# Kernel optimization log

Hardware: AMD Instinct MI355X
Metric: run time of the kernel (lower is better)

Reference implementation:

```python
import jax, jax.numpy as jnp
import numpy as np

N, E, D, H, C = 40000, 640000, 128, 4, 32  # nodes, edges, in_hid, heads, out_channels/head
NUM_NODE_TYPE, NUM_EDGE_TYPE = 8, 8
NEG_SLOPE = 0.2
EDGE_TYPE_SELF = 0


def setup_inputs() -> dict:
    key = jax.random.key(0)
    ks = jax.random.split(key, 12)
    x = jax.random.normal(ks[0], (N, D), dtype=jnp.float32)
    # build edges with no self-loops (the module filters src==dst before adding self-loops)
    src = jax.random.randint(ks[1], (E,), 0, N, dtype=jnp.int32)
    off = jax.random.randint(ks[2], (E,), 1, N, dtype=jnp.int32)
    dst = (src + off) % N
    edge_index = jnp.stack([src, dst])  # [2, E]
    node_type = jax.random.randint(ks[3], (N,), 0, NUM_NODE_TYPE, dtype=jnp.int32)
    edge_type = jax.random.randint(ks[4], (E,), 0, NUM_EDGE_TYPE, dtype=jnp.int32)
    g = 0.05
    Wq = jax.random.normal(ks[5], (H * C, D), dtype=jnp.float32) * g
    Wk = jax.random.normal(ks[6], (H * C, D), dtype=jnp.float32) * g
    Wv = jax.random.normal(ks[7], (H * C, D), dtype=jnp.float32) * g
    att_i = jax.random.normal(ks[8], (1, H, C), dtype=jnp.float32) * g
    att_j = jax.random.normal(ks[9], (1, H, C), dtype=jnp.float32) * g
    bias = jnp.zeros((H * C,), dtype=jnp.float32)
    node_emb_table = jax.random.normal(ks[10], (NUM_NODE_TYPE, D), dtype=jnp.float32) * g
    edge_emb_table = jax.random.normal(ks[11], (NUM_EDGE_TYPE, D), dtype=jnp.float32) * g
    return {"x": x, "edge_index": edge_index, "node_type": node_type,
            "edge_type": edge_type, "Wq": Wq, "Wk": Wk, "Wv": Wv,
            "att_i": att_i, "att_j": att_j, "bias": bias,
            "node_emb_table": node_emb_table, "edge_emb_table": edge_emb_table}


def reference(x, edge_index, node_type, edge_type, Wq, Wk, Wv,
              att_i, att_j, bias, node_emb_table, edge_emb_table):
    n = x.shape[0]
    # node-type embedding add
    x = x + node_emb_table[node_type]                       # [N, D]
    xq = x @ Wq.T                                           # [N, H*C]
    # add self-loops (input edges contain no src==dst by construction)
    self_idx = jnp.arange(n, dtype=edge_index.dtype)
    src = jnp.concatenate([edge_index[0], self_idx])        # [E+N]
    dst = jnp.concatenate([edge_index[1], self_idx])        # [E+N]
    et = jnp.concatenate([edge_type,
                          jnp.full((n,), EDGE_TYPE_SELF, dtype=edge_type.dtype)])
    edge_emb = edge_emb_table[et]                           # [E+N, D]
    # message: per-edge gather + K/V linear + additive attention
    x_j = x[src] + edge_emb                                 # [E+N, D]
    xq_i = xq[dst].reshape(-1, H, C)                        # [E+N, H, C]
    x_k = (x_j @ Wk.T).reshape(-1, H, C)
    x_v = (x_j @ Wv.T).reshape(-1, H, C)
    alpha = (xq_i * att_i).sum(-1) + (x_k * att_j).sum(-1)  # [E+N, H]
    alpha = jax.nn.leaky_relu(alpha, NEG_SLOPE)
    # segment softmax over destination nodes (PyG softmax, eps=1e-16)
    amax = jax.ops.segment_max(alpha, dst, num_segments=n)  # [N, H]
    alpha = jnp.exp(alpha - amax[dst])
    denom = jax.ops.segment_sum(alpha, dst, num_segments=n)
    alpha = alpha / (denom[dst] + 1e-16)
    # scatter-add weighted values
    out = jax.ops.segment_sum(x_v * alpha[..., None], dst, num_segments=n)  # [N, H, C]
    return out.reshape(n, H * C) + bias
```

## Files before the change

kernel.cpp:

```cpp
#include <hip/hip_runtime.h>
#include <math.h>

#define NN 40000
#define NE 640000
#define NTOT (NE + NN)
#define D 128
#define NH 4
#define NC 32
#define NEG 0.2f

typedef __attribute__((ext_vector_type(8))) short bf16x8;
typedef __attribute__((ext_vector_type(4))) float f32x4;

__device__ __forceinline__ unsigned pack_bf16(float a, float b) {
  unsigned ua = __float_as_uint(a), ub = __float_as_uint(b);
  ua = (ua + 0x7FFFu + ((ua >> 16) & 1u)) >> 16;
  ub = (ub + 0x7FFFu + ((ub >> 16) & 1u)) & 0xFFFF0000u;
  return ub | ua;
}

__device__ __forceinline__ bf16x8 to_bf16x8(float4 a, float4 b) {
  union { bf16x8 v; unsigned u[4]; } r;
  r.u[0] = pack_bf16(a.x, a.y);
  r.u[1] = pack_bf16(a.z, a.w);
  r.u[2] = pack_bf16(b.x, b.y);
  r.u[3] = pack_bf16(b.z, b.w);
  return r.v;
}

__global__ __launch_bounds__(256) void k_tables(
    const float* __restrict__ Wq, const float* __restrict__ Wk,
    const float* __restrict__ Wv,
    const float* __restrict__ att_i, const float* __restrict__ att_j,
    const float* __restrict__ nemb, const float* __restrict__ eemb,
    float* __restrict__ ev, float* __restrict__ vemb,
    float* __restrict__ a_et, float* __restrict__ aqt, float* __restrict__ akt,
    unsigned* __restrict__ Wvh) {
  int b = blockIdx.x, t = threadIdx.x;
  if (b < 8) {
    __shared__ float er[128], nr[128];
    if (t < 128) { er[t] = eemb[b * D + t]; nr[t] = nemb[b * D + t]; }
    __syncthreads();
    int o = t & 127;
    const float* __restrict__ wr = Wv + (size_t)o * D;
    const float* src = (t < 128) ? er : nr;
    float s = 0.f;
#pragma unroll 8
    for (int d = 0; d < D; ++d) s = fmaf(wr[d], src[d], s);
    if (t < 128) ev[b * D + o] = s;
    else         vemb[b * D + o] = s;
  } else if (b == 8) {
    __shared__ float w_s[1024];
    for (int j = t; j < 1024; j += 256) {
      int isq = (j < 512);
      int h = (j >> 7) & 3, d = j & 127;
      const float* __restrict__ Wm = isq ? Wq : Wk;
      const float* __restrict__ am = isq ? att_i : att_j;
      float s = 0.f;
#pragma unroll
      for (int c = 0; c < NC; ++c) s = fmaf(am[h * NC + c], Wm[(h * NC + c) * D + d], s);
      w_s[j] = s;
    }
    __syncthreads();
    for (int j = t; j < 1024; j += 256) {
      int r = j >> 6;
      int c2 = (j & 63) * 2;
      float a = 0.f, bb = 0.f;
      if (r < 8) { a = w_s[r * 128 + c2]; bb = w_s[r * 128 + c2 + 1]; }
      Wvh[(128 + r) * 64 + (j & 63)] = pack_bf16(a, bb);
    }
    if (t < 96) {
      int grp = t >> 5, u = t & 31;
      int ty = u >> 2, hh = u & 3;
      const float* wrow = (grp == 1) ? (w_s + hh * 128) : (w_s + 512 + hh * 128);
      const float* __restrict__ emb = (grp == 0) ? (eemb + ty * D) : (nemb + ty * D);
      float s = 0.f;
#pragma unroll 8
      for (int d = 0; d < D; ++d) s = fmaf(wrow[d], emb[d], s);
      if (grp == 0)      a_et[u] = s;
      else if (grp == 1) aqt[u] = s;
      else               akt[u] = s;
    }
  } else {
    for (int j = t; j < 8192; j += 256) {
      Wvh[j] = pack_bf16(Wv[2 * j], Wv[2 * j + 1]);
    }
  }
}

__global__ void k_hist(const int* __restrict__ ei, int* __restrict__ counts,
                       int* __restrict__ rank) {
  int i = blockIdx.x * blockDim.x + threadIdx.x;
  if (i >= NE / 4) return;
  int4 d4 = ((const int4*)(ei + NE))[i];
  int4 r;
  r.x = atomicAdd(&counts[d4.x], 1);
  r.y = atomicAdd(&counts[d4.y], 1);
  r.z = atomicAdd(&counts[d4.z], 1);
  r.w = atomicAdd(&counts[d4.w], 1);
  ((int4*)rank)[i] = r;
}

__global__ __launch_bounds__(1024) void k_scan(const int* __restrict__ counts,
                                               int* __restrict__ rowptr) {
  __shared__ int wsum[16];
  int t = threadIdx.x;
  int lane = t & 63, wv = t >> 6;
  int local[40];
  int total = 0;
  if (t < 1000) {
    const int4* __restrict__ cp = (const int4*)(counts + t * 40);
#pragma unroll
    for (int j = 0; j < 10; ++j) {
      int4 c = cp[j];
      local[4 * j + 0] = total; total += c.x + 1;
      local[4 * j + 1] = total; total += c.y + 1;
      local[4 * j + 2] = total; total += c.z + 1;
      local[4 * j + 3] = total; total += c.w + 1;
    }
  }
  int inc = total;
#pragma unroll
  for (int off = 1; off < 64; off <<= 1) {
    int v = __shfl_up(inc, off, 64);
    if (lane >= off) inc += v;
  }
  if (lane == 63) wsum[wv] = inc;
  __syncthreads();
  if (wv == 0 && lane < 16) {
    int o = wsum[lane];
    int s = o;
#pragma unroll
    for (int off = 1; off < 16; off <<= 1) {
      int v = __shfl_up(s, off, 16);
      if (lane >= off) s += v;
    }
    wsum[lane] = s - o;
  }
  __syncthreads();
  int offset = wsum[wv] + inc - total;
  if (t < 1000) {
    int base = t * 40;
#pragma unroll
    for (int j = 0; j < 40; ++j) rowptr[base + j] = offset + local[j];
    if (t == 999) rowptr[NN] = offset + total;
  }
}

__global__ void k_scatter(const int* __restrict__ ei, const int* __restrict__ etype,
                          const int* __restrict__ rowptr, const int* __restrict__ rank,
                          unsigned* __restrict__ packed) {
  int i = blockIdx.x * blockDim.x + threadIdx.x;
  if (i < NE / 4) {
    int4 s4 = ((const int4*)ei)[i];
    int4 d4 = ((const int4*)(ei + NE))[i];
    int4 t4 = ((const int4*)etype)[i];
    int4 r4 = ((const int4*)rank)[i];
    packed[rowptr[d4.x] + r4.x] = (unsigned)s4.x | ((unsigned)t4.x << 16);
    packed[rowptr[d4.y] + r4.y] = (unsigned)s4.y | ((unsigned)t4.y << 16);
    packed[rowptr[d4.z] + r4.z] = (unsigned)s4.z | ((unsigned)t4.z << 16);
    packed[rowptr[d4.w] + r4.w] = (unsigned)s4.w | ((unsigned)t4.w << 16);
  } else if (i < NE / 4 + NN) {
    int n = i - NE / 4;
    packed[rowptr[n + 1] - 1] = (unsigned)n;
  }
}

__global__ __launch_bounds__(256) void k_xv(const float* __restrict__ x,
        const int* __restrict__ node_type, const unsigned* __restrict__ Wvh,
        const float* __restrict__ vemb,
        const float* __restrict__ aqt, const float* __restrict__ akt,
        unsigned* __restrict__ xvh, float* __restrict__ aq, float* __restrict__ ak) {
  int t = threadIdx.x;
  int w = t >> 6, l = t & 63;
  int quad = l >> 4, col = l & 15;
  int n0w = blockIdx.x * 64 + w * 16;
  const float4* __restrict__ xr = (const float4*)(x + (size_t)(n0w + col) * D);
  bf16x8 afr[4];
#pragma unroll
  for (int s = 0; s < 4; ++s) {
    const float4* p = xr + s * 8 + quad * 2;
    afr[s] = to_bf16x8(p[0], p[1]);
  }
  f32x4 acc[9];
#pragma unroll
  for (int ct = 0; ct < 9; ++ct) acc[ct] = (f32x4){0.f, 0.f, 0.f, 0.f};
#pragma unroll
  for (int ct = 0; ct < 9; ++ct) {
    const unsigned* __restrict__ brow = Wvh + (size_t)(ct * 16 + col) * 64;
#pragma unroll
    for (int s = 0; s < 4; ++s) {
      bf16x8 bfr = *(const bf16x8*)(brow + s * 16 + quad * 4);
      acc[ct] = __builtin_amdgcn_mfma_f32_16x16x32_bf16(afr[s], bfr, acc[ct], 0, 0, 0);
    }
  }
  int nodes[4]; int ntv[4];
#pragma unroll
  for (int r = 0; r < 4; ++r) {
    nodes[r] = n0w + quad * 4 + r;
    ntv[r] = node_type[nodes[r]];
  }
#pragma unroll
  for (int ct = 0; ct < 8; ++ct) {
    int c = ct * 16 + col;
#pragma unroll
    for (int r = 0; r < 4; ++r) {
      float val = acc[ct][r] + vemb[ntv[r] * D + c];
      float pv = __shfl_xor(val, 1);
      if (!(col & 1)) {
        xvh[nodes[r] * 64 + ct * 8 + (col >> 1)] = pack_bf16(val, pv);
      }
    }
  }
  if (col < 4) {
#pragma unroll
    for (int r = 0; r < 4; ++r)
      aq[nodes[r] * NH + col] = acc[8][r] + aqt[ntv[r] * NH + col];
  } else if (col < 8) {
#pragma unroll
    for (int r = 0; r < 4; ++r)
      ak[nodes[r] * NH + (col - 4)] = acc[8][r] + akt[ntv[r] * NH + (col - 4)];
  }
}

__global__ __launch_bounds__(256) void k_gather(const int* __restrict__ rowptr,
        const unsigned* __restrict__ packed,
        const float* __restrict__ aq, const float* __restrict__ ak,
        const float* __restrict__ a_et, const unsigned* __restrict__ xvh,
        const float* __restrict__ ev, const float* __restrict__ bias,
        float* __restrict__ out) {
  int n = (int)((blockIdx.x * blockDim.x + threadIdx.x) >> 6);
  int l = threadIdx.x & 63;
  if (n >= NN) return;
  int g = l >> 4, q = l & 15;
  int h = q >> 2;
  float aqh = aq[n * NH + h];
  int e0 = rowptr[n], e1 = rowptr[n + 1];
  const uint4* __restrict__ xv4 = (const uint4*)xvh;
  float acc0 = 0.f, acc1 = 0.f, acc2 = 0.f, acc3 = 0.f;
  float acc4 = 0.f, acc5 = 0.f, acc6 = 0.f, acc7 = 0.f, dsum = 0.f;
  int deg = e1 - e0;
  int iters = (deg + 3) >> 2;
  int e = e0 + g;
  bool val = (e < e1);
  unsigned rec = packed[val ? e : e0];
  int src = (int)(rec & 0xFFFFu), et = (int)(rec >> 16);
  float sA = ak[src * NH + h] + a_et[et * NH + h];
  uint4 vb = xv4[src * 16 + q];
  const float* evp = ev + et * D + 8 * q;
  float4 ea = *(const float4*)evp, eb = *(const float4*)(evp + 4);
  for (int it = 0; it < iters; ++it) {
    int e2 = e + 4;
    bool v2 = (e2 < e1);
    float sA2 = 0.f; uint4 vb2 = make_uint4(0, 0, 0, 0);
    float4 ea2 = make_float4(0.f, 0.f, 0.f, 0.f);
    float4 eb2 = make_float4(0.f, 0.f, 0.f, 0.f);
    if (it + 1 < iters) {
      unsigned rec2 = packed[v2 ? e2 : e0];
      int s2 = (int)(rec2 & 0xFFFFu), t2 = (int)(rec2 >> 16);
      sA2 = ak[s2 * NH + h] + a_et[t2 * NH + h];
      vb2 = xv4[s2 * 16 + q];
      const float* ep2 = ev + t2 * D + 8 * q;
      ea2 = *(const float4*)ep2; eb2 = *(const float4*)(ep2 + 4);
    }
    float s = aqh + sA;
    s = (s > 0.f) ? s : NEG * s;
    float p = val ? __expf(s) : 0.f;
    float f0 = __uint_as_float(vb.x << 16);
    float f1 = __uint_as_float(vb.x & 0xFFFF0000u);
    float f2 = __uint_as_float(vb.y << 16);
    float f3 = __uint_as_float(vb.y & 0xFFFF0000u);
    float f4 = __uint_as_float(vb.z << 16);
    float f5 = __uint_as_float(vb.z & 0xFFFF0000u);
    float f6 = __uint_as_float(vb.w << 16);
    float f7 = __uint_as_float(vb.w & 0xFFFF0000u);
    acc0 = fmaf(p, f0 + ea.x, acc0);
    acc1 = fmaf(p, f1 + ea.y, acc1);
    acc2 = fmaf(p, f2 + ea.z, acc2);
    acc3 = fmaf(p, f3 + ea.w, acc3);
    acc4 = fmaf(p, f4 + eb.x, acc4);
    acc5 = fmaf(p, f5 + eb.y, acc5);
    acc6 = fmaf(p, f6 + eb.z, acc6);
    acc7 = fmaf(p, f7 + eb.w, acc7);
    dsum += p;
    e = e2; val = v2; sA = sA2; vb = vb2; ea = ea2; eb = eb2;
  }
  acc0 += __shfl_xor(acc0, 16); acc0 += __shfl_xor(acc0, 32);
  acc1 += __shfl_xor(acc1, 16); acc1 += __shfl_xor(acc1, 32);
  acc2 += __shfl_xor(acc2, 16); acc2 += __shfl_xor(acc2, 32);
  acc3 += __shfl_xor(acc3, 16); acc3 += __shfl_xor(acc3, 32);
  acc4 += __shfl_xor(acc4, 16); acc4 += __shfl_xor(acc4, 32);
  acc5 += __shfl_xor(acc5, 16); acc5 += __shfl_xor(acc5, 32);
  acc6 += __shfl_xor(acc6, 16); acc6 += __shfl_xor(acc6, 32);
  acc7 += __shfl_xor(acc7, 16); acc7 += __shfl_xor(acc7, 32);
  dsum += __shfl_xor(dsum, 16); dsum += __shfl_xor(dsum, 32);
  if (g == 0) {
    float inv = 1.f / (dsum + 1e-16f);
    const float4 b0 = *(const float4*)(bias + 8 * q);
    const float4 b1 = *(const float4*)(bias + 8 * q + 4);
    float4 o0 = make_float4(acc0 * inv + b0.x, acc1 * inv + b0.y,
                            acc2 * inv + b0.z, acc3 * inv + b0.w);
    float4 o1 = make_float4(acc4 * inv + b1.x, acc5 * inv + b1.y,
                            acc6 * inv + b1.z, acc7 * inv + b1.w);
    float4* op = (float4*)(out + (size_t)n * D + 8 * q);
    op[0] = o0; op[1] = o1;
  }
}

extern "C" void kernel_launch(void* const* d_in, const int* in_sizes, int n_in,
                              void* d_out, int out_size, void* d_ws, size_t ws_size,
                              hipStream_t stream) {
  const float* x      = (const float*)d_in[0];
  const int*   ei     = (const int*)d_in[1];
  const int*   ntype  = (const int*)d_in[2];
  const int*   etype  = (const int*)d_in[3];
  const float* Wq     = (const float*)d_in[4];
  const float* Wk     = (const float*)d_in[5];
  const float* Wv     = (const float*)d_in[6];
  const float* att_i  = (const float*)d_in[7];
  const float* att_j  = (const float*)d_in[8];
  const float* bias   = (const float*)d_in[9];
  const float* nemb   = (const float*)d_in[10];
  const float* eemb   = (const float*)d_in[11];
  float* out = (float*)d_out;

  float* ws     = (float*)d_ws;
  unsigned* xvh = (unsigned*)ws;
  float* aq     = ws + (size_t)NN * 64;
  float* ak     = aq + NN * NH;
  float* ev     = ak + NN * NH;
  float* vemb   = ev + 1024;
  float* a_et   = vemb + 1024;
  float* aqt    = a_et + 32;
  float* akt    = aqt + 32;
  unsigned* Wvh = (unsigned*)(akt + 32);
  int*   counts = (int*)(Wvh + 9216);
  int*   rowptr = counts + NN;
  int*   rank   = rowptr + NN + 16;
  unsigned* packed = (unsigned*)(rank + NE);

  hipMemsetAsync(counts, 0, NN * sizeof(int), stream);
  k_tables<<<dim3(10), dim3(256), 0, stream>>>(Wq, Wk, Wv, att_i, att_j, nemb, eemb,
                                               ev, vemb, a_et, aqt, akt, Wvh);
  k_hist<<<dim3((NE / 4 + 255) / 256), dim3(256), 0, stream>>>(ei, counts, rank);
  k_scan<<<dim3(1), dim3(1024), 0, stream>>>(counts, rowptr);
  k_scatter<<<dim3((NE / 4 + NN + 255) / 256), dim3(256), 0, stream>>>(ei, etype, rowptr, rank, packed);
  k_xv<<<dim3(625), dim3(256), 0, stream>>>(x, ntype, Wvh, vemb, aqt, akt, xvh, aq, ak);
  k_gather<<<dim3((NN + 3) / 4), dim3(256), 0, stream>>>(rowptr, packed, aq, ak, a_et,
                                                         xvh, ev, bias, out);
}
```

Before: 205.8 us.

## Fuse CSR build into one cooperative kernel and widen gather per-lane columns

Merges the table setup, counts memset, histogram, scan and scatter into a single cooperative kernel with grid-wide syncs, replacing five launches and a memset with one launch. The scan now runs in one 256-thread block over chunks. The gather kernel also switches to 8 lanes per edge with 16 columns each and 8 edges in flight per iteration, aiming for more memory parallelism per warp. The costs are serialization across grid barriers, a slower single-block scan, and higher register pressure in the gather.

```diff
diff --git a/kernel.cpp b/kernel.cpp
--- a/kernel.cpp
+++ b/kernel.cpp
@@ -1,5 +1,8 @@
 #include <hip/hip_runtime.h>
+#include <hip/hip_cooperative_groups.h>
 #include <math.h>
+
+namespace cg = cooperative_groups;
 
 #define NN 40000
 #define NE 640000
@@ -8,6 +11,7 @@
 #define NH 4
 #define NC 32
 #define NEG 0.2f
+#define NBLK 512
 
 typedef __attribute__((ext_vector_type(8))) short bf16x8;
 typedef __attribute__((ext_vector_type(4))) float f32x4;
@@ -28,29 +32,35 @@
   return r.v;
 }
 
-__global__ __launch_bounds__(256) void k_tables(
+__global__ __launch_bounds__(256) void k_build(
     const float* __restrict__ Wq, const float* __restrict__ Wk,
     const float* __restrict__ Wv,
     const float* __restrict__ att_i, const float* __restrict__ att_j,
     const float* __restrict__ nemb, const float* __restrict__ eemb,
+    const int* __restrict__ ei, const int* __restrict__ etype,
     float* __restrict__ ev, float* __restrict__ vemb,
     float* __restrict__ a_et, float* __restrict__ aqt, float* __restrict__ akt,
-    unsigned* __restrict__ Wvh) {
+    unsigned* __restrict__ Wvh, int* __restrict__ counts,
+    int* __restrict__ rank, int* __restrict__ rowptr,
+    unsigned* __restrict__ packed) {
+  cg::grid_group grid = cg::this_grid();
+  __shared__ float sm[1024];
   int b = blockIdx.x, t = threadIdx.x;
+  int gtid = b * 256 + t;
+  int gsz = NBLK * 256;
+
   if (b < 8) {
-    __shared__ float er[128], nr[128];
-    if (t < 128) { er[t] = eemb[b * D + t]; nr[t] = nemb[b * D + t]; }
+    if (t < 128) { sm[t] = eemb[b * D + t]; sm[128 + t] = nemb[b * D + t]; }
     __syncthreads();
     int o = t & 127;
     const float* __restrict__ wr = Wv + (size_t)o * D;
-    const float* src = (t < 128) ? er : nr;
+    const float* src = (t < 128) ? sm : (sm + 128);
     float s = 0.f;
 #pragma unroll 8
     for (int d = 0; d < D; ++d) s = fmaf(wr[d], src[d], s);
     if (t < 128) ev[b * D + o] = s;
     else         vemb[b * D + o] = s;
   } else if (b == 8) {
-    __shared__ float w_s[1024];
     for (int j = t; j < 1024; j += 256) {
       int isq = (j < 512);
       int h = (j >> 7) & 3, d = j & 127;
@@ -59,20 +69,20 @@
       float s = 0.f;
 #pragma unroll
       for (int c = 0; c < NC; ++c) s = fmaf(am[h * NC + c], Wm[(h * NC + c) * D + d], s);
-      w_s[j] = s;
+      sm[j] = s;
     }
     __syncthreads();
     for (int j = t; j < 1024; j += 256) {
       int r = j >> 6;
       int c2 = (j & 63) * 2;
       float a = 0.f, bb = 0.f;
-      if (r < 8) { a = w_s[r * 128 + c2]; bb = w_s[r * 128 + c2 + 1]; }
+      if (r < 8) { a = sm[r * 128 + c2]; bb = sm[r * 128 + c2 + 1]; }
       Wvh[(128 + r) * 64 + (j & 63)] = pack_bf16(a, bb);
     }
     if (t < 96) {
       int grp = t >> 5, u = t & 31;
       int ty = u >> 2, hh = u & 3;
-      const float* wrow = (grp == 1) ? (w_s + hh * 128) : (w_s + 512 + hh * 128);
+      const float* wrow = (grp == 1) ? (sm + hh * 128) : (sm + 512 + hh * 128);
       const float* __restrict__ emb = (grp == 0) ? (eemb + ty * D) : (nemb + ty * D);
       float s = 0.f;
 #pragma unroll 8
@@ -81,88 +91,84 @@
       else if (grp == 1) aqt[u] = s;
       else               akt[u] = s;
     }
-  } else {
+  } else if (b == 9) {
     for (int j = t; j < 8192; j += 256) {
       Wvh[j] = pack_bf16(Wv[2 * j], Wv[2 * j + 1]);
     }
-  }
-}
-
-__global__ void k_hist(const int* __restrict__ ei, int* __restrict__ counts,
-                       int* __restrict__ rank) {
-  int i = blockIdx.x * blockDim.x + threadIdx.x;
-  if (i >= NE / 4) return;
-  int4 d4 = ((const int4*)(ei + NE))[i];
-  int4 r;
-  r.x = atomicAdd(&counts[d4.x], 1);
-  r.y = atomicAdd(&counts[d4.y], 1);
-  r.z = atomicAdd(&counts[d4.z], 1);
-  r.w = atomicAdd(&counts[d4.w], 1);
-  ((int4*)rank)[i] = r;
-}
-
-__global__ __launch_bounds__(1024) void k_scan(const int* __restrict__ counts,
-                                               int* __restrict__ rowptr) {
-  __shared__ int wsum[16];
-  int t = threadIdx.x;
-  int lane = t & 63, wv = t >> 6;
-  int local[40];
-  int total = 0;
-  if (t < 1000) {
-    const int4* __restrict__ cp = (const int4*)(counts + t * 40);
-#pragma unroll
-    for (int j = 0; j < 10; ++j) {
-      int4 c = cp[j];
-      local[4 * j + 0] = total; total += c.x + 1;
-      local[4 * j + 1] = total; total += c.y + 1;
-      local[4 * j + 2] = total; total += c.z + 1;
-      local[4 * j + 3] = total; total += c.w + 1;
-    }
-  }
-  int inc = total;
-#pragma unroll
-  for (int off = 1; off < 64; off <<= 1) {
-    int v = __shfl_up(inc, off, 64);
-    if (lane >= off) inc += v;
-  }
-  if (lane == 63) wsum[wv] = inc;
-  __syncthreads();
-  if (wv == 0 && lane < 16) {
-    int o = wsum[lane];
-    int s = o;
-#pragma unroll
-    for (int off = 1; off < 16; off <<= 1) {
-      int v = __shfl_up(s, off, 16);
-      if (lane >= off) s += v;
-    }
-    wsum[lane] = s - o;
-  }
-  __syncthreads();
-  int offset = wsum[wv] + inc - total;
-  if (t < 1000) {
-    int base = t * 40;
-#pragma unroll
-    for (int j = 0; j < 40; ++j) rowptr[base + j] = offset + local[j];
-    if (t == 999) rowptr[NN] = offset + total;
-  }
-}
-
-__global__ void k_scatter(const int* __restrict__ ei, const int* __restrict__ etype,
-                          const int* __restrict__ rowptr, const int* __restrict__ rank,
-                          unsigned* __restrict__ packed) {
-  int i = blockIdx.x * blockDim.x + threadIdx.x;
-  if (i < NE / 4) {
-    int4 s4 = ((const int4*)ei)[i];
+  } else {
+    for (int i = (b - 10) * 256 + t; i < NN; i += (NBLK - 10) * 256) counts[i] = 0;
+  }
+  grid.sync();
+
+  for (int i = gtid; i < NE / 4; i += gsz) {
     int4 d4 = ((const int4*)(ei + NE))[i];
-    int4 t4 = ((const int4*)etype)[i];
-    int4 r4 = ((const int4*)rank)[i];
-    packed[rowptr[d4.x] + r4.x] = (unsigned)s4.x | ((unsigned)t4.x << 16);
-    packed[rowptr[d4.y] + r4.y] = (unsigned)s4.y | ((unsigned)t4.y << 16);
-    packed[rowptr[d4.z] + r4.z] = (unsigned)s4.z | ((unsigned)t4.z << 16);
-    packed[rowptr[d4.w] + r4.w] = (unsigned)s4.w | ((unsigned)t4.w << 16);
-  } else if (i < NE / 4 + NN) {
-    int n = i - NE / 4;
-    packed[rowptr[n + 1] - 1] = (unsigned)n;
+    int4 r;
+    r.x = atomicAdd(&counts[d4.x], 1);
+    r.y = atomicAdd(&counts[d4.y], 1);
+    r.z = atomicAdd(&counts[d4.z], 1);
+    r.w = atomicAdd(&counts[d4.w], 1);
+    ((int4*)rank)[i] = r;
+  }
+  grid.sync();
+
+  if (b == 0) {
+    int* si = (int*)sm;
+    if (t == 0) si[4] = 0;
+    __syncthreads();
+    int lane = t & 63, wv = t >> 6;
+    for (int chunk = 0; chunk < NN; chunk += 4096) {
+      int base_i = chunk + t * 16;
+      bool in = (base_i < NN);
+      int local[16]; int tot = 0;
+      if (in) {
+        const int4* __restrict__ cp = (const int4*)(counts + base_i);
+#pragma unroll
+        for (int j4 = 0; j4 < 4; ++j4) {
+          int4 c = cp[j4];
+          local[4 * j4 + 0] = tot; tot += c.x + 1;
+          local[4 * j4 + 1] = tot; tot += c.y + 1;
+          local[4 * j4 + 2] = tot; tot += c.z + 1;
+          local[4 * j4 + 3] = tot; tot += c.w + 1;
+        }
+      }
+      int inc = tot;
+#pragma unroll
+      for (int off = 1; off < 64; off <<= 1) {
+        int v = __shfl_up(inc, off, 64);
+        if (lane >= off) inc += v;
+      }
+      if (lane == 63) si[wv] = inc;
+      __syncthreads();
+      int woff = 0;
+      for (int w2 = 0; w2 < wv; ++w2) woff += si[w2];
+      int off0 = si[4] + woff + inc - tot;
+      if (in) {
+#pragma unroll
+        for (int k = 0; k < 16; ++k) rowptr[base_i + k] = off0 + local[k];
+      }
+      int csum = si[0] + si[1] + si[2] + si[3];
+      __syncthreads();
+      if (t == 0) si[4] += csum;
+      __syncthreads();
+    }
+    if (t == 0) rowptr[NN] = si[4];
+  }
+  grid.sync();
+
+  for (int i = gtid; i < NE / 4 + NN; i += gsz) {
+    if (i < NE / 4) {
+      int4 s4 = ((const int4*)ei)[i];
+      int4 d4 = ((const int4*)(ei + NE))[i];
+      int4 t4 = ((const int4*)etype)[i];
+      int4 r4 = ((const int4*)rank)[i];
+      packed[rowptr[d4.x] + r4.x] = (unsigned)s4.x | ((unsigned)t4.x << 16);
+      packed[rowptr[d4.y] + r4.y] = (unsigned)s4.y | ((unsigned)t4.y << 16);
+      packed[rowptr[d4.z] + r4.z] = (unsigned)s4.z | ((unsigned)t4.z << 16);
+      packed[rowptr[d4.w] + r4.w] = (unsigned)s4.w | ((unsigned)t4.w << 16);
+    } else {
+      int n = i - NE / 4;
+      packed[rowptr[n + 1] - 1] = (unsigned)n;
+    }
   }
 }
 
@@ -232,78 +238,94 @@
   int n = (int)((blockIdx.x * blockDim.x + threadIdx.x) >> 6);
   int l = threadIdx.x & 63;
   if (n >= NN) return;
-  int g = l >> 4, q = l & 15;
-  int h = q >> 2;
+  int g = l >> 3, q = l & 7;
+  int h = q >> 1;
   float aqh = aq[n * NH + h];
   int e0 = rowptr[n], e1 = rowptr[n + 1];
   const uint4* __restrict__ xv4 = (const uint4*)xvh;
-  float acc0 = 0.f, acc1 = 0.f, acc2 = 0.f, acc3 = 0.f;
-  float acc4 = 0.f, acc5 = 0.f, acc6 = 0.f, acc7 = 0.f, dsum = 0.f;
-  int deg = e1 - e0;
-  int iters = (deg + 3) >> 2;
+  float acc[16];
+#pragma unroll
+  for (int k = 0; k < 16; ++k) acc[k] = 0.f;
+  float dsum = 0.f;
+  int iters = (e1 - e0 + 7) >> 3;
   int e = e0 + g;
   bool val = (e < e1);
   unsigned rec = packed[val ? e : e0];
   int src = (int)(rec & 0xFFFFu), et = (int)(rec >> 16);
   float sA = ak[src * NH + h] + a_et[et * NH + h];
-  uint4 vb = xv4[src * 16 + q];
-  const float* evp = ev + et * D + 8 * q;
-  float4 ea = *(const float4*)evp, eb = *(const float4*)(evp + 4);
+  uint4 vb0 = xv4[src * 16 + 2 * q];
+  uint4 vb1 = xv4[src * 16 + 2 * q + 1];
+  const float4* __restrict__ ep = (const float4*)(ev + et * D + 16 * q);
+  float4 ea0 = ep[0], ea1 = ep[1], ea2 = ep[2], ea3 = ep[3];
   for (int it = 0; it < iters; ++it) {
-    int e2 = e + 4;
+    int e2 = e + 8;
     bool v2 = (e2 < e1);
-    float sA2 = 0.f; uint4 vb2 = make_uint4(0, 0, 0, 0);
-    float4 ea2 = make_float4(0.f, 0.f, 0.f, 0.f);
-    float4 eb2 = make_float4(0.f, 0.f, 0.f, 0.f);
+    float sAn = 0.f;
+    uint4 vb0n = make_uint4(0, 0, 0, 0), vb1n = make_uint4(0, 0, 0, 0);
+    float4 ea0n = make_float4(0.f, 0.f, 0.f, 0.f), ea1n = ea0n, ea2n = ea0n, ea3n = ea0n;
     if (it + 1 < iters) {
       unsigned rec2 = packed[v2 ? e2 : e0];
       int s2 = (int)(rec2 & 0xFFFFu), t2 = (int)(rec2 >> 16);
-      sA2 = ak[s2 * NH + h] + a_et[t2 * NH + h];
-      vb2 = xv4[s2 * 16 + q];
-      const float* ep2 = ev + t2 * D + 8 * q;
-      ea2 = *(const float4*)ep2; eb2 = *(const float4*)(ep2 + 4);
+      sAn = ak[s2 * NH + h] + a_et[t2 * NH + h];
+      vb0n = xv4[s2 * 16 + 2 * q];
+      vb1n = xv4[s2 * 16 + 2 * q + 1];
+      const float4* __restrict__ ep2 = (const float4*)(ev + t2 * D + 16 * q);
+      ea0n = ep2[0]; ea1n = ep2[1]; ea2n = ep2[2]; ea3n = ep2[3];
     }
     float s = aqh + sA;
     s = (s > 0.f) ? s : NEG * s;
     float p = val ? __expf(s) : 0.f;
-    float f0 = __uint_as_float(vb.x << 16);
-    float f1 = __uint_as_float(vb.x & 0xFFFF0000u);
-    float f2 = __uint_as_float(vb.y << 16);
-    float f3 = __uint_as_float(vb.y & 0xFFFF0000u);
-    float f4 = __uint_as_float(vb.z << 16);
-    float f5 = __uint_as_float(vb.z & 0xFFFF0000u);
-    float f6 = __uint_as_float(vb.w << 16);
-    float f7 = __uint_as_float(vb.w & 0xFFFF0000u);
-    acc0 = fmaf(p, f0 + ea.x, acc0);
-    acc1 = fmaf(p, f1 + ea.y, acc1);
-    acc2 = fmaf(p, f2 + ea.z, acc2);
-    acc3 = fmaf(p, f3 + ea.w, acc3);
-    acc4 = fmaf(p, f4 + eb.x, acc4);
-    acc5 = fmaf(p, f5 + eb.y, acc5);
-    acc6 = fmaf(p, f6 + eb.z, acc6);
-    acc7 = fmaf(p, f7 + eb.w, acc7);
+    float f[16];
+    f[0]  = __uint_as_float(vb0.x << 16); f[1]  = __uint_as_float(vb0.x & 0xFFFF0000u);
+    f[2]  = __uint_as_float(vb0.y << 16); f[3]  = __uint_as_float(vb0.y & 0xFFFF0000u);
+    f[4]  = __uint_as_float(vb0.z << 16); f[5]  = __uint_as_float(vb0.z & 0xFFFF0000u);
+    f[6]  = __uint_as_float(vb0.w << 16); f[7]  = __uint_as_float(vb0.w & 0xFFFF0000u);
+    f[8]  = __uint_as_float(vb1.x << 16); f[9]  = __uint_as_float(vb1.x & 0xFFFF0000u);
+    f[10] = __uint_as_float(vb1.y << 16); f[11] = __uint_as_float(vb1.y & 0xFFFF0000u);
+    f[12] = __uint_as_float(vb1.z << 16); f[13] = __uint_as_float(vb1.z & 0xFFFF0000u);
+    f[14] = __uint_as_float(vb1.w << 16); f[15] = __uint_as_float(vb1.w & 0xFFFF0000u);
+    acc[0]  = fmaf(p, f[0]  + ea0.x, acc[0]);
+    acc[1]  = fmaf(p, f[1]  + ea0.y, acc[1]);
+    acc[2]  = fmaf(p, f[2]  + ea0.z, acc[2]);
+    acc[3]  = fmaf(p, f[3]  + ea0.w, acc[3]);
+    acc[4]  = fmaf(p, f[4]  + ea1.x, acc[4]);
+    acc[5]  = fmaf(p, f[5]  + ea1.y, acc[5]);
+    acc[6]  = fmaf(p, f[6]  + ea1.z, acc[6]);
+    acc[7]  = fmaf(p, f[7]  + ea1.w, acc[7]);
+    acc[8]  = fmaf(p, f[8]  + ea2.x, acc[8]);
+    acc[9]  = fmaf(p, f[9]  + ea2.y, acc[9]);
+    acc[10] = fmaf(p, f[10] + ea2.z, acc[10]);
+    acc[11] = fmaf(p, f[11] + ea2.w, acc[11]);
+    acc[12] = fmaf(p, f[12] + ea3.x, acc[12]);
+    acc[13] = fmaf(p, f[13] + ea3.y, acc[13]);
+    acc[14] = fmaf(p, f[14] + ea3.z, acc[14]);
+    acc[15] = fmaf(p, f[15] + ea3.w, acc[15]);
     dsum += p;
-    e = e2; val = v2; sA = sA2; vb = vb2; ea = ea2; eb = eb2;
-  }
-  acc0 += __shfl_xor(acc0, 16); acc0 += __shfl_xor(acc0, 32);
-  acc1 += __shfl_xor(acc1, 16); acc1 += __shfl_xor(acc1, 32);
-  acc2 += __shfl_xor(acc2, 16); acc2 += __shfl_xor(acc2, 32);
-  acc3 += __shfl_xor(acc3, 16); acc3 += __shfl_xor(acc3, 32);
-  acc4 += __shfl_xor(acc4, 16); acc4 += __shfl_xor(acc4, 32);
-  acc5 += __shfl_xor(acc5, 16); acc5 += __shfl_xor(acc5, 32);
-  acc6 += __shfl_xor(acc6, 16); acc6 += __shfl_xor(acc6, 32);
-  acc7 += __shfl_xor(acc7, 16); acc7 += __shfl_xor(acc7, 32);
-  dsum += __shfl_xor(dsum, 16); dsum += __shfl_xor(dsum, 32);
+    e = e2; val = v2; sA = sAn;
+    vb0 = vb0n; vb1 = vb1n;
+    ea0 = ea0n; ea1 = ea1n; ea2 = ea2n; ea3 = ea3n;
+  }
+#pragma unroll
+  for (int k = 0; k < 16; ++k) {
+    acc[k] += __shfl_xor(acc[k], 8);
+    acc[k] += __shfl_xor(acc[k], 16);
+    acc[k] += __shfl_xor(acc[k], 32);
+  }
+  dsum += __shfl_xor(dsum, 8);
+  dsum += __shfl_xor(dsum, 16);
+  dsum += __shfl_xor(dsum, 32);
   if (g == 0) {
     float inv = 1.f / (dsum + 1e-16f);
-    const float4 b0 = *(const float4*)(bias + 8 * q);
-    const float4 b1 = *(const float4*)(bias + 8 * q + 4);
-    float4 o0 = make_float4(acc0 * inv + b0.x, acc1 * inv + b0.y,
-                            acc2 * inv + b0.z, acc3 * inv + b0.w);
-    float4 o1 = make_float4(acc4 * inv + b1.x, acc5 * inv + b1.y,
-                            acc6 * inv + b1.z, acc7 * inv + b1.w);
-    float4* op = (float4*)(out + (size_t)n * D + 8 * q);
-    op[0] = o0; op[1] = o1;
+    const float4* __restrict__ b4 = (const float4*)(bias + 16 * q);
+    float4* __restrict__ op = (float4*)(out + (size_t)n * D + 16 * q);
+#pragma unroll
+    for (int k4 = 0; k4 < 4; ++k4) {
+      float4 bb = b4[k4];
+      op[k4] = make_float4(acc[4 * k4 + 0] * inv + bb.x,
+                           acc[4 * k4 + 1] * inv + bb.y,
+                           acc[4 * k4 + 2] * inv + bb.z,
+                           acc[4 * k4 + 3] * inv + bb.w);
+    }
   }
 }
 
@@ -339,12 +361,14 @@
   int*   rank   = rowptr + NN + 16;
   unsigned* packed = (unsigned*)(rank + NE);
 
-  hipMemsetAsync(counts, 0, NN * sizeof(int), stream);
-  k_tables<<<dim3(10), dim3(256), 0, stream>>>(Wq, Wk, Wv, att_i, att_j, nemb, eemb,
-                                               ev, vemb, a_et, aqt, akt, Wvh);
-  k_hist<<<dim3((NE / 4 + 255) / 256), dim3(256), 0, stream>>>(ei, counts, rank);
-  k_scan<<<dim3(1), dim3(1024), 0, stream>>>(counts, rowptr);
-  k_scatter<<<dim3((NE / 4 + NN + 255) / 256), dim3(256), 0, stream>>>(ei, etype, rowptr, rank, packed);
+  void* kb_args[] = {
+    (void*)&Wq, (void*)&Wk, (void*)&Wv, (void*)&att_i, (void*)&att_j,
+    (void*)&nemb, (void*)&eemb, (void*)&ei, (void*)&etype,
+    (void*)&ev, (void*)&vemb, (void*)&a_et, (void*)&aqt, (void*)&akt,
+    (void*)&Wvh, (void*)&counts, (void*)&rank, (void*)&rowptr, (void*)&packed
+  };
+  hipLaunchCooperativeKernel((const void*)k_build, dim3(NBLK), dim3(256),
+                             kb_args, 0, stream);
   k_xv<<<dim3(625), dim3(256), 0, stream>>>(x, ntype, Wvh, vemb, aqt, akt, xvh, aq, ak);
   k_gather<<<dim3((NN + 3) / 4), dim3(256), 0, stream>>>(rowptr, packed, aq, ak, a_et,
                                                          xvh, ev, bias, out);
```

After: 402.3 us. 1.95x slower.
